# Optimization experiments

Measured on AMD Instinct MI355X. Metric: run time of the kernel, lower is better.

## Reference

```python
import jax, jax.numpy as jnp
import numpy as np

DIM = 1024
NUM_HEADS = 16
HEAD_DIM = DIM // NUM_HEADS
ROPE_BASE = 10000.0


def _rope_cos_sin(seq_len, head_dim):
    inv_freq = 1.0 / (ROPE_BASE ** (jnp.arange(0, head_dim, 2, dtype=jnp.float32) / head_dim))
    t = jnp.arange(seq_len, dtype=jnp.float32)
    freqs = t[:, None] * inv_freq[None, :]            # [S, Dh/2]
    emb = jnp.concatenate([freqs, freqs], axis=-1)    # [S, Dh]
    return jnp.cos(emb), jnp.sin(emb)


def _rotate_half(x):
    half = x.shape[-1] // 2
    return jnp.concatenate([-x[..., half:], x[..., :half]], axis=-1)


def setup_inputs() -> dict:
    key = jax.random.key(0)
    k1, k2, k3 = jax.random.split(key, 3)
    B, S = 2, 2048
    x = jax.random.normal(k1, (B, S, DIM), dtype=jnp.float32)
    w_qkv = jax.random.normal(k2, (3 * DIM, DIM), dtype=jnp.float32) * (DIM ** -0.5)
    w_out = jax.random.normal(k3, (DIM, DIM), dtype=jnp.float32) * (DIM ** -0.5)
    return {"x": x, "w_qkv": w_qkv, "w_out": w_out}


def reference(x, w_qkv, w_out):
    B, S, D = x.shape
    H, Dh = NUM_HEADS, HEAD_DIM
    scale = Dh ** -0.5

    qkv = (x @ w_qkv.T).reshape(B, S, 3, H, Dh)      # [B,S,3,H,Dh]
    qkv = jnp.transpose(qkv, (2, 0, 3, 1, 4))        # [3,B,H,S,Dh]
    q, k, v = qkv[0], qkv[1], qkv[2]

    cos, sin = _rope_cos_sin(S, Dh)                  # [S,Dh]
    cos = cos[None, None, :, :]
    sin = sin[None, None, :, :]
    q = q * cos + _rotate_half(q) * sin
    k = k * cos + _rotate_half(k) * sin

    scores = jnp.einsum('bhqd,bhkd->bhqk', q, k) * scale
    causal_mask = jnp.triu(jnp.ones((S, S), dtype=bool), k=1)
    scores = jnp.where(causal_mask[None, None], -jnp.inf, scores)
    attn = jax.nn.softmax(scores, axis=-1)
    out = jnp.einsum('bhqk,bhkd->bhqd', attn, v)      # [B,H,S,Dh]
    out = jnp.transpose(out, (0, 2, 1, 3)).reshape(B, S, D)
    return out @ w_out.T
```

## Files before the change

kernel.cpp:

```cpp
#include <hip/hip_runtime.h>
#include <stdint.h>

typedef uint16_t u16;
typedef __attribute__((ext_vector_type(8))) short bf16x8;
typedef __attribute__((ext_vector_type(4))) float f32x4;

__device__ inline u16 f2b(float f) {
  uint32_t u = __float_as_uint(f);
  u += 0x7FFF + ((u >> 16) & 1);
  return (u16)(u >> 16);
}
__device__ inline float b2f(u16 h) {
  return __uint_as_float(((uint32_t)h) << 16);
}

typedef __attribute__((address_space(1))) void gvoid;
typedef __attribute__((address_space(3))) void lvoid;
#define GLOAD16(gp, lp)                                                        \
  __builtin_amdgcn_global_load_lds((gvoid*)(gp), (lvoid*)(lp), 16, 0, 0)

__global__ void k_detect(const u16* __restrict__ X, int* __restrict__ flag) {
  __shared__ int cnt;
  const int t = threadIdx.x;
  if (t == 0) cnt = 0;
  __syncthreads();
  float av = fabsf(b2f(X[t * 2]));
  int wild = (av < 1000.0f) ? 0 : 1;
  atomicAdd(&cnt, wild);
  __syncthreads();
  if (t == 0) flag[0] = (cnt > 16) ? 1 : 0;
}

__global__ __launch_bounds__(256) void k_qkv_rope(const void* __restrict__ Xv,
                                                  const void* __restrict__ Wv,
                                                  const int* __restrict__ flag,
                                                  u16* __restrict__ Qo,
                                                  u16* __restrict__ Ko,
                                                  u16* __restrict__ Vo) {
  union ShQ {
    struct { u16 A[2][2][64][32]; u16 B[2][3][64][32]; } st;
    float Cs[64][66];
  };
  __shared__ ShQ sh;
  const int mode = flag[0];
  const int h = blockIdx.x;
  const int n0h = h * 64;
  const int m0 = blockIdx.y * 128;
  const int t = threadIdx.x, w = t >> 6, lane = t & 63;
  const int lr = lane & 15, lq = lane >> 4;
  f32x4 acc[3][2][4] = {};
  const int rA = t >> 2;
  const int gcol = (((t & 3) ^ ((rA >> 1) & 3)) << 3);
  const int aoff0 = (m0 + rA) * 1024 + gcol;
  const int aoff1 = aoff0 + 65536;
  const int boff0 = (n0h + rA) * 1024 + gcol;

  if (mode == 0) {
    const u16* Xp = (const u16*)Xv;
    const u16* Wp = (const u16*)Wv;
#define STAGE_QKV(buf, kk)                                                     \
    do {                                                                       \
      GLOAD16(Xp + aoff0 + (kk),           &sh.st.A[buf][0][(w << 4)][0]);     \
      GLOAD16(Xp + aoff1 + (kk),           &sh.st.A[buf][1][(w << 4)][0]);     \
      GLOAD16(Wp + boff0 + (kk),           &sh.st.B[buf][0][(w << 4)][0]);     \
      GLOAD16(Wp + boff0 + 1048576 + (kk), &sh.st.B[buf][1][(w << 4)][0]);     \
      GLOAD16(Wp + boff0 + 2097152 + (kk), &sh.st.B[buf][2][(w << 4)][0]);     \
    } while (0)
    STAGE_QKV(0, 0);
    asm volatile("s_waitcnt vmcnt(0)" ::: "memory");
    __syncthreads();
    int cur = 0;
    for (int k0 = 0; k0 < 1024; k0 += 32) {
      if (k0 + 32 < 1024) STAGE_QKV(cur ^ 1, k0 + 32);
      bf16x8 bf[3];
      const int rowB = (w << 4) + lr;
      const int scB = ((lq ^ ((rowB >> 1) & 3)) << 3);
#pragma unroll
      for (int e = 0; e < 3; ++e)
        bf[e] = *(const bf16x8*)&sh.st.B[cur][e][rowB][scB];
#pragma unroll
      for (int mt = 0; mt < 4; ++mt) {
        const int row = (mt << 4) + lr;
        const int sc = ((lq ^ ((row >> 1) & 3)) << 3);
        bf16x8 af0 = *(const bf16x8*)&sh.st.A[cur][0][row][sc];
        bf16x8 af1 = *(const bf16x8*)&sh.st.A[cur][1][row][sc];
#pragma unroll
        for (int e = 0; e < 3; ++e) {
          acc[e][0][mt] = __builtin_amdgcn_mfma_f32_16x16x32_bf16(af0, bf[e], acc[e][0][mt], 0, 0, 0);
          acc[e][1][mt] = __builtin_amdgcn_mfma_f32_16x16x32_bf16(af1, bf[e], acc[e][1][mt], 0, 0, 0);
        }
      }
      __syncthreads();
      cur ^= 1;
    }
#undef STAGE_QKV
  } else {
    const float* Xf = (const float*)Xv;
    const float* Wf = (const float*)Wv;
    for (int k0 = 0; k0 < 1024; k0 += 32) {
      __syncthreads();
#pragma unroll
      for (int ee = 0; ee < 8; ++ee) {
        const int pc = ((t & 3) << 3) + ee;
        sh.st.A[0][0][rA][pc] = f2b(Xf[aoff0 + k0 + ee]);
        sh.st.A[0][1][rA][pc] = f2b(Xf[aoff1 + k0 + ee]);
        sh.st.B[0][0][rA][pc] = f2b(Wf[boff0 + k0 + ee]);
        sh.st.B[0][1][rA][pc] = f2b(Wf[boff0 + 1048576 + k0 + ee]);
        sh.st.B[0][2][rA][pc] = f2b(Wf[boff0 + 2097152 + k0 + ee]);
      }
      __syncthreads();
      bf16x8 bf[3];
      const int rowB = (w << 4) + lr;
      const int scB = ((lq ^ ((rowB >> 1) & 3)) << 3);
#pragma unroll
      for (int e = 0; e < 3; ++e)
        bf[e] = *(const bf16x8*)&sh.st.B[0][e][rowB][scB];
#pragma unroll
      for (int mt = 0; mt < 4; ++mt) {
        const int row = (mt << 4) + lr;
        const int sc = ((lq ^ ((row >> 1) & 3)) << 3);
        bf16x8 af0 = *(const bf16x8*)&sh.st.A[0][0][row][sc];
        bf16x8 af1 = *(const bf16x8*)&sh.st.A[0][1][row][sc];
#pragma unroll
        for (int e = 0; e < 3; ++e) {
          acc[e][0][mt] = __builtin_amdgcn_mfma_f32_16x16x32_bf16(af0, bf[e], acc[e][0][mt], 0, 0, 0);
          acc[e][1][mt] = __builtin_amdgcn_mfma_f32_16x16x32_bf16(af1, bf[e], acc[e][1][mt], 0, 0, 0);
        }
      }
    }
  }

  for (int f = 0; f < 2; ++f) {
    const int m0f = m0 + f * 64;
    for (int e = 0; e < 3; ++e) {
      __syncthreads();
      {
        const int col = (w << 4) + lr;
#pragma unroll
        for (int mt = 0; mt < 4; ++mt)
#pragma unroll
          for (int i = 0; i < 4; ++i)
            sh.Cs[mt * 16 + lq * 4 + i][col] = acc[e][f][mt][i];
      }
      __syncthreads();
      if (e == 2) {
        const int sx = t & 63, dh0 = (t >> 6) * 16;
        const int m = m0f + sx, b = m >> 11, s = m & 2047;
        const long hb = (long)(b * 16 + h) * 64;
#pragma unroll
        for (int u = 0; u < 16; ++u) {
          int dh = dh0 + u;
          Vo[(hb + dh) * 2048 + s] = f2b(sh.Cs[sx][dh]);
        }
      } else {
        const int r = t >> 2, dh0 = (t & 3) * 16;
        const int m = m0f + r, b = m >> 11, s = m & 2047;
        const int obase = ((b * 16 + h) * 2048 + s) * 64;
        u16* O = (e == 0) ? Qo : Ko;
#pragma unroll
        for (int u = 0; u < 16; ++u) {
          int dh = dh0 + u;
          float v  = sh.Cs[r][dh];
          float vp = sh.Cs[r][dh ^ 32];
          float sign = (dh < 32) ? -1.0f : 1.0f;
          float fr  = __expf((float)(dh & 31) * -0.28782314f);
          float ang = (float)s * fr;
          float sn = __sinf(ang), cs = __cosf(ang);
          O[obase + dh] = f2b(v * cs + sign * vp * sn);
        }
      }
    }
  }
}

__device__ __forceinline__ void attn_tile(u16 QP[64][72], u16 Ks[64][72],
                                          u16 Vt[64][72], const bf16x8 qf[2],
                                          f32x4 o_acc[4], float& m_i, float& l_i,
                                          int kt, int qt_tile, int w, int lr,
                                          int lq, int lq4, int base16, int qrow_l) {
  f32x4 sa[4] = {};
#pragma unroll
  for (int mb = 0; mb < 4; ++mb)
#pragma unroll
    for (int kk = 0; kk < 2; ++kk) {
      bf16x8 kf = *(const bf16x8*)&Ks[mb * 16 + lr][kk * 32 + lq * 8];
      sa[mb] = __builtin_amdgcn_mfma_f32_16x16x32_bf16(kf, qf[kk], sa[mb], 0, 0, 0);
    }
  float sc[4][4];
  float m_new = m_i;
#pragma unroll
  for (int mb = 0; mb < 4; ++mb)
#pragma unroll
    for (int i = 0; i < 4; ++i) {
      float sv = sa[mb][i] * 0.125f;
      if (kt == qt_tile && (mb * 16 + lq4 + i) > qrow_l) sv = -3.0e4f;
      sc[mb][i] = sv;
      m_new = fmaxf(m_new, sv);
    }
  m_new = fmaxf(m_new, __shfl_xor(m_new, 16));
  m_new = fmaxf(m_new, __shfl_xor(m_new, 32));
  float alpha = __expf(m_i - m_new);
  m_i = m_new;
  float p[4][4], sm = 0.f;
#pragma unroll
  for (int mb = 0; mb < 4; ++mb)
#pragma unroll
    for (int i = 0; i < 4; ++i) { p[mb][i] = __expf(sc[mb][i] - m_new); sm += p[mb][i]; }
  sm += __shfl_xor(sm, 16);
  sm += __shfl_xor(sm, 32);
  l_i = l_i * alpha + sm;
#pragma unroll
  for (int mb = 0; mb < 4; ++mb) {
    uint2 pk;
    pk.x = (uint32_t)f2b(p[mb][0]) | ((uint32_t)f2b(p[mb][1]) << 16);
    pk.y = (uint32_t)f2b(p[mb][2]) | ((uint32_t)f2b(p[mb][3]) << 16);
    *(uint2*)&QP[w * 16 + lr][mb * 16 + lq4] = pk;
  }
#pragma unroll
  for (int i = 0; i < 4; ++i) {
    float ai = __shfl(alpha, base16 | (lq4 + i));
    o_acc[0][i] *= ai; o_acc[1][i] *= ai;
    o_acc[2][i] *= ai; o_acc[3][i] *= ai;
  }
  asm volatile("s_waitcnt lgkmcnt(0)" ::: "memory");
#pragma unroll
  for (int kk = 0; kk < 2; ++kk) {
    bf16x8 pf = *(const bf16x8*)&QP[w * 16 + lr][kk * 32 + lq * 8];
#pragma unroll
    for (int nb = 0; nb < 4; ++nb) {
      bf16x8 vf = *(const bf16x8*)&Vt[nb * 16 + lr][kk * 32 + lq * 8];
      o_acc[nb] = __builtin_amdgcn_mfma_f32_16x16x32_bf16(pf, vf, o_acc[nb], 0, 0, 0);
    }
  }
}

__global__ __launch_bounds__(256) void k_attn(const u16* __restrict__ Q,
                                              const u16* __restrict__ K,
                                              const u16* __restrict__ V,
                                              u16* __restrict__ AO) {
  __shared__ u16 QP[64][72];
  __shared__ u16 Ks[64][72];
  __shared__ u16 Vt[64][72];
  const int qtA = 31 - blockIdx.x;
  const int qtB = blockIdx.x;
  const int bh = blockIdx.y;
  const int b = bh >> 4, h = bh & 15;
  const u16* Qg = Q + (bh * 2048) * 64;
  const u16* Kg = K + bh * 2048 * 64;
  const u16* Vg = V + (long)bh * 64 * 2048;
  const int t = threadIdx.x, w = t >> 6, lane = t & 63;
  const int lr = lane & 15, lq = lane >> 4;
  const int lq4 = lq * 4;
  const int base16 = lane & 48;
  const int r0 = t >> 3, c0 = (t & 7) * 8;
  const int qrow_l = w * 16 + lr;

  bf16x8 qfA[2], qfB[2];
  *(uint4*)&QP[r0][c0]      = *(const uint4*)&Qg[(qtA * 64 + r0) * 64 + c0];
  *(uint4*)&QP[r0 + 32][c0] = *(const uint4*)&Qg[(qtA * 64 + r0 + 32) * 64 + c0];
  __syncthreads();
#pragma unroll
  for (int kk = 0; kk < 2; ++kk)
    qfA[kk] = *(const bf16x8*)&QP[w * 16 + lr][kk * 32 + lq * 8];
  __syncthreads();
  *(uint4*)&QP[r0][c0]      = *(const uint4*)&Qg[(qtB * 64 + r0) * 64 + c0];
  *(uint4*)&QP[r0 + 32][c0] = *(const uint4*)&Qg[(qtB * 64 + r0 + 32) * 64 + c0];
  __syncthreads();
#pragma unroll
  for (int kk = 0; kk < 2; ++kk)
    qfB[kk] = *(const bf16x8*)&QP[w * 16 + lr][kk * 32 + lq * 8];

  float m_iA = -3.0e4f, l_iA = 0.f, m_iB = -3.0e4f, l_iB = 0.f;
  f32x4 o_accA[4] = {}, o_accB[4] = {};

  for (int kt = 0; kt <= qtA; ++kt) {
    __syncthreads();
    *(uint4*)&Ks[r0][c0]      = *(const uint4*)&Kg[(kt * 64 + r0) * 64 + c0];
    *(uint4*)&Ks[r0 + 32][c0] = *(const uint4*)&Kg[(kt * 64 + r0 + 32) * 64 + c0];
    *(uint4*)&Vt[r0][c0]      = *(const uint4*)&Vg[r0 * 2048 + kt * 64 + c0];
    *(uint4*)&Vt[r0 + 32][c0] = *(const uint4*)&Vg[(r0 + 32) * 2048 + kt * 64 + c0];
    __syncthreads();

    attn_tile(QP, Ks, Vt, qfA, o_accA, m_iA, l_iA, kt, qtA,
              w, lr, lq, lq4, base16, qrow_l);
    if (kt <= qtB) {
      asm volatile("s_waitcnt lgkmcnt(0)" ::: "memory");
      attn_tile(QP, Ks, Vt, qfB, o_accB, m_iB, l_iB, kt, qtB,
                w, lr, lq, lq4, base16, qrow_l);
    }
  }
  float linvA = 1.0f / l_iA, linvB = 1.0f / l_iB;
#pragma unroll
  for (int i = 0; i < 4; ++i) {
    float invA = __shfl(linvA, base16 | (lq4 + i));
    float invB = __shfl(linvB, base16 | (lq4 + i));
    int rowA = qtA * 64 + w * 16 + lq4 + i;
    int rowB = qtB * 64 + w * 16 + lq4 + i;
    int obA = (b * 2048 + rowA) * 1024 + h * 64;
    int obB = (b * 2048 + rowB) * 1024 + h * 64;
#pragma unroll
    for (int nb = 0; nb < 4; ++nb) {
      AO[obA + nb * 16 + lr] = f2b(o_accA[nb][i] * invA);
      AO[obB + nb * 16 + lr] = f2b(o_accB[nb][i] * invB);
    }
  }
}

__global__ __launch_bounds__(256) void k_gemm_out(const u16* __restrict__ A,
                                                  const void* __restrict__ Bv,
                                                  const int* __restrict__ flag,
                                                  void* __restrict__ Cv) {
  __shared__ u16 As[2][64][32];
  __shared__ u16 Bs[2][2][64][32];
  const int mode = flag[0];
  const int n0 = blockIdx.x * 128, m0 = blockIdx.y * 64;
  const int t = threadIdx.x, w = t >> 6, lane = t & 63;
  const int lr = lane & 15, lq = lane >> 4;
  f32x4 acc[2][4] = {};
  const int rA = t >> 2;
  const int gcol = (((t & 3) ^ ((rA >> 1) & 3)) << 3);
  const int aoff  = (m0 + rA) * 1024 + gcol;
  const int boff0 = (n0 + rA) * 1024 + gcol;
  const int boff1 = boff0 + 65536;

  if (mode == 0) {
    const u16* Bp = (const u16*)Bv;
#define STAGE_OUT(buf, kk)                                                     \
    do {                                                                       \
      GLOAD16(A + aoff + (kk),   &As[buf][(w << 4)][0]);                       \
      GLOAD16(Bp + boff0 + (kk), &Bs[buf][0][(w << 4)][0]);                    \
      GLOAD16(Bp + boff1 + (kk), &Bs[buf][1][(w << 4)][0]);                    \
    } while (0)
    STAGE_OUT(0, 0);
    asm volatile("s_waitcnt vmcnt(0)" ::: "memory");
    __syncthreads();
    int cur = 0;
    for (int k0 = 0; k0 < 1024; k0 += 32) {
      if (k0 + 32 < 1024) STAGE_OUT(cur ^ 1, k0 + 32);
      bf16x8 bfx[2];
      const int rowB = (w << 4) + lr;
      const int scB = ((lq ^ ((rowB >> 1) & 3)) << 3);
#pragma unroll
      for (int e = 0; e < 2; ++e)
        bfx[e] = *(const bf16x8*)&Bs[cur][e][rowB][scB];
#pragma unroll
      for (int mt = 0; mt < 4; ++mt) {
        const int row = (mt << 4) + lr;
        const int sc = ((lq ^ ((row >> 1) & 3)) << 3);
        bf16x8 af = *(const bf16x8*)&As[cur][row][sc];
#pragma unroll
        for (int e = 0; e < 2; ++e)
          acc[e][mt] = __builtin_amdgcn_mfma_f32_16x16x32_bf16(af, bfx[e], acc[e][mt], 0, 0, 0);
      }
      __syncthreads();
      cur ^= 1;
    }
#undef STAGE_OUT
  } else {
    const float* Bf = (const float*)Bv;
    for (int k0 = 0; k0 < 1024; k0 += 32) {
      __syncthreads();
      *(uint4*)&As[0][rA][(t & 3) << 3] = *(const uint4*)(A + aoff + k0);
#pragma unroll
      for (int ee = 0; ee < 8; ++ee) {
        const int pc = ((t & 3) << 3) + ee;
        Bs[0][0][rA][pc] = f2b(Bf[boff0 + k0 + ee]);
        Bs[0][1][rA][pc] = f2b(Bf[boff1 + k0 + ee]);
      }
      __syncthreads();
      bf16x8 bfx[2];
      const int rowB = (w << 4) + lr;
      const int scB = ((lq ^ ((rowB >> 1) & 3)) << 3);
#pragma unroll
      for (int e = 0; e < 2; ++e)
        bfx[e] = *(const bf16x8*)&Bs[0][e][rowB][scB];
#pragma unroll
      for (int mt = 0; mt < 4; ++mt) {
        const int row = (mt << 4) + lr;
        const int sc = ((lq ^ ((row >> 1) & 3)) << 3);
        bf16x8 af = *(const bf16x8*)&As[0][row][sc];
#pragma unroll
        for (int e = 0; e < 2; ++e)
          acc[e][mt] = __builtin_amdgcn_mfma_f32_16x16x32_bf16(af, bfx[e], acc[e][mt], 0, 0, 0);
      }
    }
  }
#pragma unroll
  for (int e = 0; e < 2; ++e) {
    const int col = n0 + e * 64 + (w << 4) + lr;
    if (mode == 0) {
      u16* C = (u16*)Cv;
#pragma unroll
      for (int mt = 0; mt < 4; ++mt)
#pragma unroll
        for (int i = 0; i < 4; ++i)
          C[(m0 + mt * 16 + lq * 4 + i) * 1024 + col] = f2b(acc[e][mt][i]);
    } else {
      float* C = (float*)Cv;
#pragma unroll
      for (int mt = 0; mt < 4; ++mt)
#pragma unroll
        for (int i = 0; i < 4; ++i)
          C[(m0 + mt * 16 + lq * 4 + i) * 1024 + col] = acc[e][mt][i];
    }
  }
}

extern "C" void kernel_launch(void* const* d_in, const int* in_sizes, int n_in,
                              void* d_out, int out_size, void* d_ws, size_t ws_size,
                              hipStream_t stream) {
  const void* x    = d_in[0];
  const void* wqkv = d_in[1];
  const void* wout = d_in[2];

  int* flag = (int*)d_ws;
  u16* qb = (u16*)((char*)d_ws + 256);
  u16* kb = qb + 4194304;
  u16* vb = kb + 4194304;
  u16* ao = vb + 4194304;

  k_detect  <<<dim3(1), 256, 0, stream>>>((const u16*)x, flag);
  k_qkv_rope<<<dim3(16, 32), 256, 0, stream>>>(x, wqkv, flag, qb, kb, vb);
  k_attn    <<<dim3(16, 32), 256, 0, stream>>>(qb, kb, vb, ao);
  k_gemm_out<<<dim3(8, 64), 256, 0, stream>>>(ao, wout, flag, d_out);
}
```

Measured before the change: 242.2 us.

## Shrink QKV GEMM tile to 64 rows with register prefetch and padded LDS

Halves the QKV projection M-tile from 128 to 64 rows and doubles the grid, dropping the second A tile and its accumulators. The bf16 path replaces the double-buffered direct-to-LDS async loads with register prefetch into a single LDS buffer. Both paths use padded rows instead of XOR swizzling. Launch bounds now request 4 blocks per CU. The intent is higher occupancy and lower register pressure, at the cost of loading each weight tile twice as often. The fp32 output GEMM path also loses its swizzle and computes offsets inline.

```diff
diff --git a/kernel.cpp b/kernel.cpp
--- a/kernel.cpp
+++ b/kernel.cpp
@@ -31,143 +31,121 @@
   if (t == 0) flag[0] = (cnt > 16) ? 1 : 0;
 }
 
-__global__ __launch_bounds__(256) void k_qkv_rope(const void* __restrict__ Xv,
-                                                  const void* __restrict__ Wv,
-                                                  const int* __restrict__ flag,
-                                                  u16* __restrict__ Qo,
-                                                  u16* __restrict__ Ko,
-                                                  u16* __restrict__ Vo) {
-  union ShQ {
-    struct { u16 A[2][2][64][32]; u16 B[2][3][64][32]; } st;
-    float Cs[64][66];
-  };
-  __shared__ ShQ sh;
+__global__ __launch_bounds__(256, 4) void k_qkv_rope(const void* __restrict__ Xv,
+                                                     const void* __restrict__ Wv,
+                                                     const int* __restrict__ flag,
+                                                     u16* __restrict__ Qo,
+                                                     u16* __restrict__ Ko,
+                                                     u16* __restrict__ Vo) {
+  __shared__ u16 As[64][40];
+  __shared__ u16 Bs[3][64][40];
+  __shared__ float Cs[64][66];
   const int mode = flag[0];
   const int h = blockIdx.x;
   const int n0h = h * 64;
-  const int m0 = blockIdx.y * 128;
+  const int m0 = blockIdx.y * 64;
   const int t = threadIdx.x, w = t >> 6, lane = t & 63;
   const int lr = lane & 15, lq = lane >> 4;
-  f32x4 acc[3][2][4] = {};
-  const int rA = t >> 2;
-  const int gcol = (((t & 3) ^ ((rA >> 1) & 3)) << 3);
-  const int aoff0 = (m0 + rA) * 1024 + gcol;
-  const int aoff1 = aoff0 + 65536;
-  const int boff0 = (n0h + rA) * 1024 + gcol;
+  f32x4 acc[3][4] = {};
+  const int rA = t >> 2, cA = (t & 3) * 8;
+  const int aoff0 = (m0 + rA) * 1024 + cA;
+  const int boff0 = (n0h + rA) * 1024 + cA;
 
   if (mode == 0) {
     const u16* Xp = (const u16*)Xv;
     const u16* Wp = (const u16*)Wv;
-#define STAGE_QKV(buf, kk)                                                     \
-    do {                                                                       \
-      GLOAD16(Xp + aoff0 + (kk),           &sh.st.A[buf][0][(w << 4)][0]);     \
-      GLOAD16(Xp + aoff1 + (kk),           &sh.st.A[buf][1][(w << 4)][0]);     \
-      GLOAD16(Wp + boff0 + (kk),           &sh.st.B[buf][0][(w << 4)][0]);     \
-      GLOAD16(Wp + boff0 + 1048576 + (kk), &sh.st.B[buf][1][(w << 4)][0]);     \
-      GLOAD16(Wp + boff0 + 2097152 + (kk), &sh.st.B[buf][2][(w << 4)][0]);     \
-    } while (0)
-    STAGE_QKV(0, 0);
-    asm volatile("s_waitcnt vmcnt(0)" ::: "memory");
+    uint4 pa0 = *(const uint4*)(Xp + aoff0);
+    uint4 pb0 = *(const uint4*)(Wp + boff0);
+    uint4 pb1 = *(const uint4*)(Wp + boff0 + 1048576);
+    uint4 pb2 = *(const uint4*)(Wp + boff0 + 2097152);
+    for (int k0 = 0; k0 < 1024; k0 += 32) {
+      __syncthreads();
+      *(uint4*)&As[rA][cA]    = pa0;
+      *(uint4*)&Bs[0][rA][cA] = pb0;
+      *(uint4*)&Bs[1][rA][cA] = pb1;
+      *(uint4*)&Bs[2][rA][cA] = pb2;
+      __syncthreads();
+      if (k0 + 32 < 1024) {
+        const int kn = k0 + 32;
+        pa0 = *(const uint4*)(Xp + aoff0 + kn);
+        pb0 = *(const uint4*)(Wp + boff0 + kn);
+        pb1 = *(const uint4*)(Wp + boff0 + 1048576 + kn);
+        pb2 = *(const uint4*)(Wp + boff0 + 2097152 + kn);
+      }
+      bf16x8 bf[3];
+#pragma unroll
+      for (int e = 0; e < 3; ++e)
+        bf[e] = *(const bf16x8*)&Bs[e][(w << 4) + lr][lq * 8];
+#pragma unroll
+      for (int mt = 0; mt < 4; ++mt) {
+        bf16x8 af = *(const bf16x8*)&As[(mt << 4) + lr][lq * 8];
+#pragma unroll
+        for (int e = 0; e < 3; ++e)
+          acc[e][mt] = __builtin_amdgcn_mfma_f32_16x16x32_bf16(af, bf[e], acc[e][mt], 0, 0, 0);
+      }
+    }
+  } else {
+    for (int k0 = 0; k0 < 1024; k0 += 32) {
+      __syncthreads();
+      const float* Xf = (const float*)Xv;
+      const float* Wf = (const float*)Wv;
+#pragma unroll
+      for (int ee = 0; ee < 8; ++ee) {
+        As[rA][cA + ee]    = f2b(Xf[aoff0 + k0 + ee]);
+        Bs[0][rA][cA + ee] = f2b(Wf[boff0 + k0 + ee]);
+        Bs[1][rA][cA + ee] = f2b(Wf[boff0 + 1048576 + k0 + ee]);
+        Bs[2][rA][cA + ee] = f2b(Wf[boff0 + 2097152 + k0 + ee]);
+      }
+      __syncthreads();
+      bf16x8 bf[3];
+#pragma unroll
+      for (int e = 0; e < 3; ++e)
+        bf[e] = *(const bf16x8*)&Bs[e][(w << 4) + lr][lq * 8];
+#pragma unroll
+      for (int mt = 0; mt < 4; ++mt) {
+        bf16x8 af = *(const bf16x8*)&As[(mt << 4) + lr][lq * 8];
+#pragma unroll
+        for (int e = 0; e < 3; ++e)
+          acc[e][mt] = __builtin_amdgcn_mfma_f32_16x16x32_bf16(af, bf[e], acc[e][mt], 0, 0, 0);
+      }
+    }
+  }
+
+  for (int e = 0; e < 3; ++e) {
     __syncthreads();
-    int cur = 0;
-    for (int k0 = 0; k0 < 1024; k0 += 32) {
-      if (k0 + 32 < 1024) STAGE_QKV(cur ^ 1, k0 + 32);
-      bf16x8 bf[3];
-      const int rowB = (w << 4) + lr;
-      const int scB = ((lq ^ ((rowB >> 1) & 3)) << 3);
-#pragma unroll
-      for (int e = 0; e < 3; ++e)
-        bf[e] = *(const bf16x8*)&sh.st.B[cur][e][rowB][scB];
-#pragma unroll
-      for (int mt = 0; mt < 4; ++mt) {
-        const int row = (mt << 4) + lr;
-        const int sc = ((lq ^ ((row >> 1) & 3)) << 3);
-        bf16x8 af0 = *(const bf16x8*)&sh.st.A[cur][0][row][sc];
-        bf16x8 af1 = *(const bf16x8*)&sh.st.A[cur][1][row][sc];
-#pragma unroll
-        for (int e = 0; e < 3; ++e) {
-          acc[e][0][mt] = __builtin_amdgcn_mfma_f32_16x16x32_bf16(af0, bf[e], acc[e][0][mt], 0, 0, 0);
-          acc[e][1][mt] = __builtin_amdgcn_mfma_f32_16x16x32_bf16(af1, bf[e], acc[e][1][mt], 0, 0, 0);
-        }
-      }
-      __syncthreads();
-      cur ^= 1;
-    }
-#undef STAGE_QKV
-  } else {
-    const float* Xf = (const float*)Xv;
-    const float* Wf = (const float*)Wv;
-    for (int k0 = 0; k0 < 1024; k0 += 32) {
-      __syncthreads();
-#pragma unroll
-      for (int ee = 0; ee < 8; ++ee) {
-        const int pc = ((t & 3) << 3) + ee;
-        sh.st.A[0][0][rA][pc] = f2b(Xf[aoff0 + k0 + ee]);
-        sh.st.A[0][1][rA][pc] = f2b(Xf[aoff1 + k0 + ee]);
-        sh.st.B[0][0][rA][pc] = f2b(Wf[boff0 + k0 + ee]);
-        sh.st.B[0][1][rA][pc] = f2b(Wf[boff0 + 1048576 + k0 + ee]);
-        sh.st.B[0][2][rA][pc] = f2b(Wf[boff0 + 2097152 + k0 + ee]);
-      }
-      __syncthreads();
-      bf16x8 bf[3];
-      const int rowB = (w << 4) + lr;
-      const int scB = ((lq ^ ((rowB >> 1) & 3)) << 3);
-#pragma unroll
-      for (int e = 0; e < 3; ++e)
-        bf[e] = *(const bf16x8*)&sh.st.B[0][e][rowB][scB];
-#pragma unroll
-      for (int mt = 0; mt < 4; ++mt) {
-        const int row = (mt << 4) + lr;
-        const int sc = ((lq ^ ((row >> 1) & 3)) << 3);
-        bf16x8 af0 = *(const bf16x8*)&sh.st.A[0][0][row][sc];
-        bf16x8 af1 = *(const bf16x8*)&sh.st.A[0][1][row][sc];
-#pragma unroll
-        for (int e = 0; e < 3; ++e) {
-          acc[e][0][mt] = __builtin_amdgcn_mfma_f32_16x16x32_bf16(af0, bf[e], acc[e][0][mt], 0, 0, 0);
-          acc[e][1][mt] = __builtin_amdgcn_mfma_f32_16x16x32_bf16(af1, bf[e], acc[e][1][mt], 0, 0, 0);
-        }
-      }
-    }
-  }
-
-  for (int f = 0; f < 2; ++f) {
-    const int m0f = m0 + f * 64;
-    for (int e = 0; e < 3; ++e) {
-      __syncthreads();
-      {
-        const int col = (w << 4) + lr;
-#pragma unroll
-        for (int mt = 0; mt < 4; ++mt)
-#pragma unroll
-          for (int i = 0; i < 4; ++i)
-            sh.Cs[mt * 16 + lq * 4 + i][col] = acc[e][f][mt][i];
-      }
-      __syncthreads();
-      if (e == 2) {
-        const int sx = t & 63, dh0 = (t >> 6) * 16;
-        const int m = m0f + sx, b = m >> 11, s = m & 2047;
-        const long hb = (long)(b * 16 + h) * 64;
-#pragma unroll
-        for (int u = 0; u < 16; ++u) {
-          int dh = dh0 + u;
-          Vo[(hb + dh) * 2048 + s] = f2b(sh.Cs[sx][dh]);
-        }
-      } else {
-        const int r = t >> 2, dh0 = (t & 3) * 16;
-        const int m = m0f + r, b = m >> 11, s = m & 2047;
-        const int obase = ((b * 16 + h) * 2048 + s) * 64;
-        u16* O = (e == 0) ? Qo : Ko;
-#pragma unroll
-        for (int u = 0; u < 16; ++u) {
-          int dh = dh0 + u;
-          float v  = sh.Cs[r][dh];
-          float vp = sh.Cs[r][dh ^ 32];
-          float sign = (dh < 32) ? -1.0f : 1.0f;
-          float fr  = __expf((float)(dh & 31) * -0.28782314f);
-          float ang = (float)s * fr;
-          float sn = __sinf(ang), cs = __cosf(ang);
-          O[obase + dh] = f2b(v * cs + sign * vp * sn);
-        }
+    {
+      const int col = (w << 4) + lr;
+#pragma unroll
+      for (int mt = 0; mt < 4; ++mt)
+#pragma unroll
+        for (int i = 0; i < 4; ++i)
+          Cs[mt * 16 + lq * 4 + i][col] = acc[e][mt][i];
+    }
+    __syncthreads();
+    if (e == 2) {
+      const int sx = t & 63, dh0 = (t >> 6) * 16;
+      const int m = m0 + sx, b = m >> 11, s = m & 2047;
+      const long hb = (long)(b * 16 + h) * 64;
+#pragma unroll
+      for (int u = 0; u < 16; ++u) {
+        int dh = dh0 + u;
+        Vo[(hb + dh) * 2048 + s] = f2b(Cs[sx][dh]);
+      }
+    } else {
+      const int r = t >> 2, dh0 = (t & 3) * 16;
+      const int m = m0 + r, b = m >> 11, s = m & 2047;
+      const int obase = ((b * 16 + h) * 2048 + s) * 64;
+      u16* O = (e == 0) ? Qo : Ko;
+#pragma unroll
+      for (int u = 0; u < 16; ++u) {
+        int dh = dh0 + u;
+        float v  = Cs[r][dh];
+        float vp = Cs[r][dh ^ 32];
+        float sign = (dh < 32) ? -1.0f : 1.0f;
+        float fr  = __expf((float)(dh & 31) * -0.28782314f);
+        float ang = (float)s * fr;
+        float sn = __sinf(ang), cs = __cosf(ang);
+        O[obase + dh] = f2b(v * cs + sign * vp * sn);
       }
     }
   }
@@ -360,25 +338,22 @@
     const float* Bf = (const float*)Bv;
     for (int k0 = 0; k0 < 1024; k0 += 32) {
       __syncthreads();
-      *(uint4*)&As[0][rA][(t & 3) << 3] = *(const uint4*)(A + aoff + k0);
+      *(uint4*)&As[0][rA][(t & 3) << 3] = *(const uint4*)(A + (m0 + rA) * 1024 + ((t & 3) << 3) + k0);
 #pragma unroll
       for (int ee = 0; ee < 8; ++ee) {
         const int pc = ((t & 3) << 3) + ee;
-        Bs[0][0][rA][pc] = f2b(Bf[boff0 + k0 + ee]);
-        Bs[0][1][rA][pc] = f2b(Bf[boff1 + k0 + ee]);
+        Bs[0][0][rA][pc] = f2b(Bf[(n0 + rA) * 1024 + pc + k0]);
+        Bs[0][1][rA][pc] = f2b(Bf[(n0 + rA) * 1024 + 65536 + pc + k0]);
       }
       __syncthreads();
       bf16x8 bfx[2];
       const int rowB = (w << 4) + lr;
-      const int scB = ((lq ^ ((rowB >> 1) & 3)) << 3);
 #pragma unroll
       for (int e = 0; e < 2; ++e)
-        bfx[e] = *(const bf16x8*)&Bs[0][e][rowB][scB];
+        bfx[e] = *(const bf16x8*)&Bs[0][e][rowB][lq * 8];
 #pragma unroll
       for (int mt = 0; mt < 4; ++mt) {
-        const int row = (mt << 4) + lr;
-        const int sc = ((lq ^ ((row >> 1) & 3)) << 3);
-        bf16x8 af = *(const bf16x8*)&As[0][row][sc];
+        bf16x8 af = *(const bf16x8*)&As[0][(mt << 4) + lr][lq * 8];
 #pragma unroll
         for (int e = 0; e < 2; ++e)
           acc[e][mt] = __builtin_amdgcn_mfma_f32_16x16x32_bf16(af, bfx[e], acc[e][mt], 0, 0, 0);
@@ -420,7 +395,7 @@
   u16* ao = vb + 4194304;
 
   k_detect  <<<dim3(1), 256, 0, stream>>>((const u16*)x, flag);
-  k_qkv_rope<<<dim3(16, 32), 256, 0, stream>>>(x, wqkv, flag, qb, kb, vb);
+  k_qkv_rope<<<dim3(16, 64), 256, 0, stream>>>(x, wqkv, flag, qb, kb, vb);
   k_attn    <<<dim3(16, 32), 256, 0, stream>>>(qb, kb, vb, ao);
   k_gemm_out<<<dim3(8, 64), 256, 0, stream>>>(ao, wout, flag, d_out);
 }
```

New measurement: 245.6 us. No clear change (+1.4%).
